# Optimization experiments

Measured on AMD Instinct MI355X. Metric: run time of the kernel, lower is better.

Reference implementation:

```python
import jax, jax.numpy as jnp
import numpy as np

N = 10000
E = 320000
D = 256


def setup_inputs() -> dict:
    key = jax.random.key(0)
    ks = jax.random.split(key, 10)
    s = 1.0 / np.sqrt(D)
    return {
        "x0": jax.random.normal(ks[0], (N, D), jnp.float32),
        "edge_index": jax.random.randint(ks[1], (2, E), 0, N, jnp.int32),
        "W1": jax.random.normal(ks[2], (D, D), jnp.float32) * s,
        "b1": jax.random.normal(ks[3], (D,), jnp.float32) * s,
        "W2": jax.random.normal(ks[4], (D, D), jnp.float32) * s,
        "b2": jax.random.normal(ks[5], (D,), jnp.float32) * s,
        "wa1": jax.random.normal(ks[6], (D,), jnp.float32) * s,
        "ba1": jax.random.normal(ks[7], (1,), jnp.float32) * s,
        "wa2": jax.random.normal(ks[8], (D,), jnp.float32) * s,
        "ba2": jax.random.normal(ks[9], (1,), jnp.float32) * s,
    }


def reference(x0, edge_index, W1, b1, W2, b2, wa1, ba1, wa2, ba2):
    n = x0.shape[0]
    leaky = lambda v: jax.nn.leaky_relu(v, 0.2)
    x0_i = leaky(x0 @ W1 + b1)                      # [N, D]
    x0_j = leaky(x0 @ W2 + b2)                      # [N, D]
    a1 = x0_i @ wa1 + ba1[0]                        # [N]
    a2 = x0_j @ wa2 + ba2[0]                        # [N]
    row, col = edge_index[0], edge_index[1]
    # sigmoid(a_1 + a_2.T)[row, col] without the dense N x N intermediate
    att = jax.nn.sigmoid(a1[row] + a2[col])         # [E]
    msg = att[:, None] * x0_j[col]                  # [E, D]
    out = jax.ops.segment_sum(msg, row, num_segments=n)  # sparse.mm(attention, x0_j)
    return out + x0
```

## Files before the change

kernel.cpp:

```cpp
#include <hip/hip_runtime.h>
#include <math.h>

#define D 256
#define CAP 128

typedef float f32x4 __attribute__((ext_vector_type(4)));
typedef short s16x8 __attribute__((ext_vector_type(8)));
typedef unsigned short u16x8 __attribute__((ext_vector_type(8)));

static __device__ __forceinline__ unsigned short f2bf(float x) {
    union { float f; unsigned u; } v; v.f = x;
    unsigned r = v.u + 0x7fff + ((v.u >> 16) & 1);
    return (unsigned short)(r >> 16);
}

__global__ __launch_bounds__(256) void k_init(
    const float* __restrict__ x0, const float* __restrict__ W1,
    const float* __restrict__ W2, unsigned short* __restrict__ xb,
    unsigned short* __restrict__ wt, int* __restrict__ curp, int n)
{
    const int i = blockIdx.x * 256 + threadIdx.x;
    const int nx4 = n * D / 4;
    if (i < nx4) {
        f32x4 v = *(const f32x4*)&x0[(size_t)i * 4];
        ushort4 o;
        o.x = f2bf(v.x); o.y = f2bf(v.y); o.z = f2bf(v.z); o.w = f2bf(v.w);
        *(ushort4*)&xb[(size_t)i * 4] = o;
    }
    if (i < 2 * D * D) {
        int k = i >> 9;
        int j = i & 511;
        float v = (j < D) ? W1[(size_t)k * D + j] : W2[(size_t)k * D + (j - D)];
        wt[(size_t)j * D + k] = f2bf(v);
    }
    if (i < n) curp[(size_t)i << 5] = 0;
}

__global__ __launch_bounds__(256) void k_mfma_rank(
    const unsigned short* __restrict__ xb, const unsigned short* __restrict__ wt,
    const float* __restrict__ b1, const float* __restrict__ b2,
    const float* __restrict__ wa1, const float* __restrict__ wa2,
    const int* __restrict__ rows, const int* __restrict__ cols,
    int* __restrict__ curp, unsigned short* __restrict__ perm,
    unsigned char* __restrict__ x0j8, float* __restrict__ pa,
    float* __restrict__ sA, float* __restrict__ sB, int n, int e, int nrb)
{
    __shared__ float part[4][32];
    __shared__ float pmx[4][32];
    __shared__ float sscale[32];
    const int t = threadIdx.x;

    if ((int)blockIdx.x < nrb) {
        const int i0 = (blockIdx.x * 256 + t) * 8;
        if (i0 + 7 < e) {
            int4 ra = *(const int4*)&rows[i0];
            int4 rb4 = *(const int4*)&rows[i0 + 4];
            int4 ca = *(const int4*)&cols[i0];
            int4 cb4 = *(const int4*)&cols[i0 + 4];
            int s0 = atomicAdd(&curp[(size_t)ra.x << 5], 1);
            int s1 = atomicAdd(&curp[(size_t)ra.y << 5], 1);
            int s2 = atomicAdd(&curp[(size_t)ra.z << 5], 1);
            int s3 = atomicAdd(&curp[(size_t)ra.w << 5], 1);
            int s4 = atomicAdd(&curp[(size_t)rb4.x << 5], 1);
            int s5 = atomicAdd(&curp[(size_t)rb4.y << 5], 1);
            int s6 = atomicAdd(&curp[(size_t)rb4.z << 5], 1);
            int s7 = atomicAdd(&curp[(size_t)rb4.w << 5], 1);
            if (s0 < CAP) perm[(size_t)ra.x * CAP + s0] = (unsigned short)ca.x;
            if (s1 < CAP) perm[(size_t)ra.y * CAP + s1] = (unsigned short)ca.y;
            if (s2 < CAP) perm[(size_t)ra.z * CAP + s2] = (unsigned short)ca.z;
            if (s3 < CAP) perm[(size_t)ra.w * CAP + s3] = (unsigned short)ca.w;
            if (s4 < CAP) perm[(size_t)rb4.x * CAP + s4] = (unsigned short)cb4.x;
            if (s5 < CAP) perm[(size_t)rb4.y * CAP + s5] = (unsigned short)cb4.y;
            if (s6 < CAP) perm[(size_t)rb4.z * CAP + s6] = (unsigned short)cb4.z;
            if (s7 < CAP) perm[(size_t)rb4.w * CAP + s7] = (unsigned short)cb4.w;
        } else {
            for (int i = i0; i < e; ++i) {
                int r = rows[i];
                int slot = atomicAdd(&curp[(size_t)r << 5], 1);
                if (slot < CAP) perm[(size_t)r * CAP + slot] = (unsigned short)cols[i];
            }
        }
        return;
    }

    const int lane = t & 63, w = t >> 6;
    const int bid2 = blockIdx.x - nrb;
    const int bx = bid2 >> 2, by = bid2 & 3;
    const int rb = bx * 32;
    const int cb = by * 128 + w * 32;
    const int lr = lane & 15;
    const int kg = lane >> 4;

    f32x4 acc[2][2] = {};

    #pragma unroll
    for (int ks = 0; ks < 8; ++ks) {
        const int k0 = ks * 32 + kg * 8;
        s16x8 af[2], bfr[2];
        #pragma unroll
        for (int rf = 0; rf < 2; ++rf) {
            int row = rb + rf * 16 + lr; if (row >= n) row = n - 1;
            af[rf] = *(const s16x8*)&xb[(size_t)row * D + k0];
        }
        #pragma unroll
        for (int cf = 0; cf < 2; ++cf) {
            int col = cb + cf * 16 + lr;
            bfr[cf] = *(const s16x8*)&wt[(size_t)col * D + k0];
        }
        #pragma unroll
        for (int rf = 0; rf < 2; ++rf)
            #pragma unroll
            for (int cf = 0; cf < 2; ++cf)
                acc[rf][cf] = __builtin_amdgcn_mfma_f32_16x16x32_bf16(
                    af[rf], bfr[cf], acc[rf][cf], 0, 0, 0);
    }

    const bool isW2 = (by >= 2);
    const float* wav  = isW2 ? wa2 : wa1;
    const float* bias = isW2 ? b2  : b1;
    const int crel = cb - (isW2 ? D : 0);

    float bvv[2], wvv[2];
    #pragma unroll
    for (int cf = 0; cf < 2; ++cf) {
        bvv[cf] = bias[crel + cf * 16 + lr];
        wvv[cf] = wav[crel + cf * 16 + lr];
    }

    float rs[2][4] = {};
    float mx[2][4] = {};
    #pragma unroll
    for (int rf = 0; rf < 2; ++rf)
        #pragma unroll
        for (int cf = 0; cf < 2; ++cf)
            #pragma unroll
            for (int r = 0; r < 4; ++r) {
                float v = acc[rf][cf][r] + bvv[cf];
                v = (v > 0.0f) ? v : 0.2f * v;
                rs[rf][r] += v * wvv[cf];
                mx[rf][r] = fmaxf(mx[rf][r], fabsf(v));
            }

    #pragma unroll
    for (int rf = 0; rf < 2; ++rf)
        #pragma unroll
        for (int r = 0; r < 4; ++r) {
            float s = rs[rf][r], m = mx[rf][r];
            #pragma unroll
            for (int o = 1; o < 16; o <<= 1) {
                s += __shfl_xor(s, o, 64);
                m = fmaxf(m, __shfl_xor(m, o, 64));
            }
            if (lr == 0) {
                const int ri = rf * 16 + kg * 4 + r;
                part[w][ri] = s;
                pmx[w][ri] = m;
            }
        }
    __syncthreads();
    if (t < 32) {
        const int row = rb + t;
        float smax = fmaxf(fmaxf(pmx[0][t], pmx[1][t]),
                           fmaxf(pmx[2][t], pmx[3][t]));
        smax = fmaxf(smax, 1e-20f);
        float sc = smax * (1.0f / 127.0f);
        sscale[t] = sc;
        if (row < n) {
            pa[((size_t)row << 2) + by] =
                part[0][t] + part[1][t] + part[2][t] + part[3][t];
            if (by == 2) sA[row] = sc;
            else if (by == 3) sB[row] = sc;
        }
    }
    __syncthreads();

    if (isW2) {
        #pragma unroll
        for (int rf = 0; rf < 2; ++rf)
            #pragma unroll
            for (int r = 0; r < 4; ++r) {
                const int ri = rf * 16 + kg * 4 + r;
                const int row = rb + ri;
                if (row >= n) continue;
                const float inv_s = 1.0f / sscale[ri];
                #pragma unroll
                for (int cf = 0; cf < 2; ++cf) {
                    const int col = crel + cf * 16 + lr;
                    float v = acc[rf][cf][r] + bvv[cf];
                    v = (v > 0.0f) ? v : 0.2f * v;
                    int qv = (int)rintf(v * inv_s) + 128;
                    qv = (qv < 0) ? 0 : ((qv > 255) ? 255 : qv);
                    x0j8[(size_t)row * D + col] = (unsigned char)qv;
                }
            }
    }
}

__global__ __launch_bounds__(256) void k_agg(
    const unsigned char* __restrict__ x0j8, const float* __restrict__ x0,
    const float* __restrict__ pa, const float* __restrict__ sA,
    const float* __restrict__ sB, const float* __restrict__ ba1,
    const float* __restrict__ ba2, const int* __restrict__ curp,
    const unsigned short* __restrict__ perm, float* __restrict__ out, int n)
{
    __shared__ unsigned short scol[4][CAP + 4];
    __shared__ float sscA[4][CAP + 4];
    __shared__ float sscB[4][CAP + 4];

    const int w = threadIdx.x >> 6, lane = threadIdx.x & 63;
    const int q = lane >> 4, hl = lane & 15;
    const int row = blockIdx.x * 4 + w;

    int deg = 0;
    f32x4 res;
    if (row < n) {
        deg = curp[(size_t)row << 5];
        if (deg > CAP) deg = CAP;
        const size_t pbase = (size_t)row * CAP;
        const float a1r = pa[(size_t)row * 4] + pa[(size_t)row * 4 + 1]
                        + ba1[0] + ba2[0];
        res = *(const f32x4*)&x0[(size_t)row * D + hl * 16 + q * 4];

        for (int i = lane; i < deg; i += 64) {
            int c = perm[pbase + i];
            scol[w][i] = (unsigned short)c;
            float2 a2p = *(const float2*)&pa[((size_t)c << 2) + 2];
            float att = 1.0f / (1.0f + __expf(-(a1r + a2p.x + a2p.y)));
            sscA[w][i] = att * sA[c];
            sscB[w][i] = att * sB[c];
        }
        if (lane < 4) {
            scol[w][deg + lane] = 0;
            sscA[w][deg + lane] = 0.0f;
            sscB[w][deg + lane] = 0.0f;
        }
    }
    __syncthreads();
    if (row >= n) return;

    const int degp = (deg + 3) & ~3;
    const bool segA = (hl < 8);

    float acc[16];
    #pragma unroll
    for (int k = 0; k < 16; ++k) acc[k] = 0.0f;
    float corr = 0.0f;

    #pragma unroll 2
    for (int j = 0; j < degp; j += 4) {
        const int idx = j + q;
        const float as = segA ? sscA[w][idx] : sscB[w][idx];
        const int   c  = scol[w][idx];
        uint4 v = *(const uint4*)&x0j8[(size_t)c * D + hl * 16];
        corr += as;
        acc[0]  += as * (float)( v.x        & 255);
        acc[1]  += as * (float)((v.x >>  8) & 255);
        acc[2]  += as * (float)((v.x >> 16) & 255);
        acc[3]  += as * (float)( v.x >> 24);
        acc[4]  += as * (float)( v.y        & 255);
        acc[5]  += as * (float)((v.y >>  8) & 255);
        acc[6]  += as * (float)((v.y >> 16) & 255);
        acc[7]  += as * (float)( v.y >> 24);
        acc[8]  += as * (float)( v.z        & 255);
        acc[9]  += as * (float)((v.z >>  8) & 255);
        acc[10] += as * (float)((v.z >> 16) & 255);
        acc[11] += as * (float)( v.z >> 24);
        acc[12] += as * (float)( v.w        & 255);
        acc[13] += as * (float)((v.w >>  8) & 255);
        acc[14] += as * (float)((v.w >> 16) & 255);
        acc[15] += as * (float)( v.w >> 24);
    }

    #pragma unroll
    for (int k = 0; k < 16; ++k) acc[k] += __shfl_xor(acc[k], 16, 64);
    corr += __shfl_xor(corr, 16, 64);
    #pragma unroll
    for (int k = 0; k < 16; ++k) acc[k] += __shfl_xor(acc[k], 32, 64);
    corr += __shfl_xor(corr, 32, 64);

    const float bias128 = 128.0f * corr;

    float s0, s1, s2, s3;
    if      (q == 0) { s0 = acc[0];  s1 = acc[1];  s2 = acc[2];  s3 = acc[3];  }
    else if (q == 1) { s0 = acc[4];  s1 = acc[5];  s2 = acc[6];  s3 = acc[7];  }
    else if (q == 2) { s0 = acc[8];  s1 = acc[9];  s2 = acc[10]; s3 = acc[11]; }
    else             { s0 = acc[12]; s1 = acc[13]; s2 = acc[14]; s3 = acc[15]; }

    const int col = hl * 16 + q * 4;
    f32x4 o;
    o.x = res.x + s0 - bias128;
    o.y = res.y + s1 - bias128;
    o.z = res.z + s2 - bias128;
    o.w = res.w + s3 - bias128;
    *(f32x4*)&out[(size_t)row * D + col] = o;
}

extern "C" void kernel_launch(void* const* d_in, const int* in_sizes, int n_in,
                              void* d_out, int out_size, void* d_ws, size_t ws_size,
                              hipStream_t stream)
{
    const float* x0  = (const float*)d_in[0];
    const int*   ei  = (const int*)d_in[1];
    const float* W1  = (const float*)d_in[2];
    const float* b1  = (const float*)d_in[3];
    const float* W2  = (const float*)d_in[4];
    const float* b2  = (const float*)d_in[5];
    const float* wa1 = (const float*)d_in[6];
    const float* ba1 = (const float*)d_in[7];
    const float* wa2 = (const float*)d_in[8];
    const float* ba2 = (const float*)d_in[9];
    float* out = (float*)d_out;

    const int n = in_sizes[0] / D;
    const int e = in_sizes[1] / 2;
    const int* rows = ei;
    const int* cols = ei + e;

    char* ws = (char*)d_ws;
    unsigned short* wt   = (unsigned short*)ws;
    unsigned short* xb   = wt + (size_t)2 * D * D;
    unsigned char*  x0j8 = (unsigned char*)(xb + (size_t)n * D);
    float* pa   = (float*)(x0j8 + (size_t)n * D);
    float* sA   = pa + (size_t)4 * n;
    float* sB   = sA + n;
    int*   curp = (int*)(sB + n);
    unsigned short* perm = (unsigned short*)(curp + (size_t)n * 32);

    const int ithreads = n * D / 4;
    k_init<<<(ithreads + 255) / 256, 256, 0, stream>>>(x0, W1, W2, xb, wt,
                                                       curp, n);
    const int gx4 = ((n + 31) / 32) * 4;
    const int nrb = (e / 8 + 255) / 256;
    k_mfma_rank<<<nrb + gx4, 256, 0, stream>>>(xb, wt, b1, b2, wa1, wa2,
                                               rows, cols, curp, perm,
                                               x0j8, pa, sA, sB, n, e, nrb);
    k_agg<<<(n + 3) / 4, 256, 0, stream>>>(x0j8, x0, pa, sA, sB, ba1, ba2,
                                           curp, perm, out, n);
}
```

Measured before the change: 63.46 us.

## Move x0 bf16 conversion into rank kernel and pack per-node attention data

Measured after the change: 65.64 us. 1.03x slower.

```diff
diff --git a/kernel.cpp b/kernel.cpp
--- a/kernel.cpp
+++ b/kernel.cpp
@@ -15,18 +15,10 @@
 }
 
 __global__ __launch_bounds__(256) void k_init(
-    const float* __restrict__ x0, const float* __restrict__ W1,
-    const float* __restrict__ W2, unsigned short* __restrict__ xb,
+    const float* __restrict__ W1, const float* __restrict__ W2,
     unsigned short* __restrict__ wt, int* __restrict__ curp, int n)
 {
     const int i = blockIdx.x * 256 + threadIdx.x;
-    const int nx4 = n * D / 4;
-    if (i < nx4) {
-        f32x4 v = *(const f32x4*)&x0[(size_t)i * 4];
-        ushort4 o;
-        o.x = f2bf(v.x); o.y = f2bf(v.y); o.z = f2bf(v.z); o.w = f2bf(v.w);
-        *(ushort4*)&xb[(size_t)i * 4] = o;
-    }
     if (i < 2 * D * D) {
         int k = i >> 9;
         int j = i & 511;
@@ -36,18 +28,12 @@
     if (i < n) curp[(size_t)i << 5] = 0;
 }
 
-__global__ __launch_bounds__(256) void k_mfma_rank(
-    const unsigned short* __restrict__ xb, const unsigned short* __restrict__ wt,
-    const float* __restrict__ b1, const float* __restrict__ b2,
-    const float* __restrict__ wa1, const float* __restrict__ wa2,
+__global__ __launch_bounds__(256) void k_conv_rank(
+    const float* __restrict__ x0, unsigned short* __restrict__ xb,
     const int* __restrict__ rows, const int* __restrict__ cols,
     int* __restrict__ curp, unsigned short* __restrict__ perm,
-    unsigned char* __restrict__ x0j8, float* __restrict__ pa,
-    float* __restrict__ sA, float* __restrict__ sB, int n, int e, int nrb)
-{
-    __shared__ float part[4][32];
-    __shared__ float pmx[4][32];
-    __shared__ float sscale[32];
+    int n, int e, int nrb)
+{
     const int t = threadIdx.x;
 
     if ((int)blockIdx.x < nrb) {
@@ -83,9 +69,31 @@
         return;
     }
 
+    const int i = ((blockIdx.x - nrb) * 256 + t) * 8;
+    const int nx = n * D;
+    if (i + 7 < nx) {
+        f32x4 v0 = *(const f32x4*)&x0[i];
+        f32x4 v1 = *(const f32x4*)&x0[i + 4];
+        u16x8 o;
+        o[0] = f2bf(v0.x); o[1] = f2bf(v0.y); o[2] = f2bf(v0.z); o[3] = f2bf(v0.w);
+        o[4] = f2bf(v1.x); o[5] = f2bf(v1.y); o[6] = f2bf(v1.z); o[7] = f2bf(v1.w);
+        *(u16x8*)&xb[i] = o;
+    }
+}
+
+__global__ __launch_bounds__(256) void k_mfma(
+    const unsigned short* __restrict__ xb, const unsigned short* __restrict__ wt,
+    const float* __restrict__ b1, const float* __restrict__ b2,
+    const float* __restrict__ wa1, const float* __restrict__ wa2,
+    unsigned char* __restrict__ x0j8, float2* __restrict__ pa12,
+    float* __restrict__ pa4, int n)
+{
+    __shared__ float part[4][32];
+    __shared__ float pmx[4][32];
+    __shared__ float sscale[32];
+    const int t = threadIdx.x;
     const int lane = t & 63, w = t >> 6;
-    const int bid2 = blockIdx.x - nrb;
-    const int bx = bid2 >> 2, by = bid2 & 3;
+    const int bx = blockIdx.x >> 2, by = blockIdx.x & 3;
     const int rb = bx * 32;
     const int cb = by * 128 + w * 32;
     const int lr = lane & 15;
@@ -160,16 +168,19 @@
     __syncthreads();
     if (t < 32) {
         const int row = rb + t;
+        float sv = part[0][t] + part[1][t] + part[2][t] + part[3][t];
         float smax = fmaxf(fmaxf(pmx[0][t], pmx[1][t]),
                            fmaxf(pmx[2][t], pmx[3][t]));
         smax = fmaxf(smax, 1e-20f);
         float sc = smax * (1.0f / 127.0f);
         sscale[t] = sc;
         if (row < n) {
-            pa[((size_t)row << 2) + by] =
-                part[0][t] + part[1][t] + part[2][t] + part[3][t];
-            if (by == 2) sA[row] = sc;
-            else if (by == 3) sB[row] = sc;
+            if (by == 0)      pa12[row].x = sv;
+            else if (by == 1) pa12[row].y = sv;
+            else if (by == 2) { pa4[((size_t)row << 2)]     = sv;
+                                pa4[((size_t)row << 2) + 2] = sc; }
+            else              { pa4[((size_t)row << 2) + 1] = sv;
+                                pa4[((size_t)row << 2) + 3] = sc; }
         }
     }
     __syncthreads();
@@ -198,10 +209,10 @@
 
 __global__ __launch_bounds__(256) void k_agg(
     const unsigned char* __restrict__ x0j8, const float* __restrict__ x0,
-    const float* __restrict__ pa, const float* __restrict__ sA,
-    const float* __restrict__ sB, const float* __restrict__ ba1,
-    const float* __restrict__ ba2, const int* __restrict__ curp,
-    const unsigned short* __restrict__ perm, float* __restrict__ out, int n)
+    const float2* __restrict__ pa12, const float* __restrict__ pa4,
+    const float* __restrict__ ba1, const float* __restrict__ ba2,
+    const int* __restrict__ curp, const unsigned short* __restrict__ perm,
+    float* __restrict__ out, int n)
 {
     __shared__ unsigned short scol[4][CAP + 4];
     __shared__ float sscA[4][CAP + 4];
@@ -217,17 +228,17 @@
         deg = curp[(size_t)row << 5];
         if (deg > CAP) deg = CAP;
         const size_t pbase = (size_t)row * CAP;
-        const float a1r = pa[(size_t)row * 4] + pa[(size_t)row * 4 + 1]
-                        + ba1[0] + ba2[0];
+        float2 p12 = pa12[row];
+        const float a1r = p12.x + p12.y + ba1[0] + ba2[0];
         res = *(const f32x4*)&x0[(size_t)row * D + hl * 16 + q * 4];
 
         for (int i = lane; i < deg; i += 64) {
             int c = perm[pbase + i];
             scol[w][i] = (unsigned short)c;
-            float2 a2p = *(const float2*)&pa[((size_t)c << 2) + 2];
-            float att = 1.0f / (1.0f + __expf(-(a1r + a2p.x + a2p.y)));
-            sscA[w][i] = att * sA[c];
-            sscB[w][i] = att * sB[c];
+            f32x4 v4 = *(const f32x4*)&pa4[(size_t)c << 2];
+            float att = 1.0f / (1.0f + __expf(-(a1r + v4.x + v4.y)));
+            sscA[w][i] = att * v4.z;
+            sscB[w][i] = att * v4.w;
         }
         if (lane < 4) {
             scol[w][deg + lane] = 0;
@@ -320,20 +331,19 @@
     unsigned short* wt   = (unsigned short*)ws;
     unsigned short* xb   = wt + (size_t)2 * D * D;
     unsigned char*  x0j8 = (unsigned char*)(xb + (size_t)n * D);
-    float* pa   = (float*)(x0j8 + (size_t)n * D);
-    float* sA   = pa + (size_t)4 * n;
-    float* sB   = sA + n;
-    int*   curp = (int*)(sB + n);
+    float*  pa4  = (float*)(x0j8 + (size_t)n * D);
+    float2* pa12 = (float2*)(pa4 + (size_t)4 * n);
+    int*    curp = (int*)(pa12 + n);
     unsigned short* perm = (unsigned short*)(curp + (size_t)n * 32);
 
-    const int ithreads = n * D / 4;
-    k_init<<<(ithreads + 255) / 256, 256, 0, stream>>>(x0, W1, W2, xb, wt,
-                                                       curp, n);
-    const int gx4 = ((n + 31) / 32) * 4;
+    const int ithreads = 2 * D * D;
+    k_init<<<(ithreads + 255) / 256, 256, 0, stream>>>(W1, W2, wt, curp, n);
     const int nrb = (e / 8 + 255) / 256;
-    k_mfma_rank<<<nrb + gx4, 256, 0, stream>>>(xb, wt, b1, b2, wa1, wa2,
-                                               rows, cols, curp, perm,
-                                               x0j8, pa, sA, sB, n, e, nrb);
-    k_agg<<<(n + 3) / 4, 256, 0, stream>>>(x0j8, x0, pa, sA, sB, ba1, ba2,
+    const int ncb = (n * D / 8 + 255) / 256;
+    k_conv_rank<<<nrb + ncb, 256, 0, stream>>>(x0, xb, rows, cols, curp, perm,
+                                               n, e, nrb);
+    dim3 mg(((n + 31) / 32) * 4);
+    k_mfma<<<mg, 256, 0, stream>>>(xb, wt, b1, b2, wa1, wa2, x0j8, pa12, pa4, n);
+    k_agg<<<(n + 3) / 4, 256, 0, stream>>>(x0j8, x0, pa12, pa4, ba1, ba2,
                                            curp, perm, out, n);
 }
```
